# Kernel optimization log

Measured on AMD Instinct MI355X. Metric: run time of the kernel, lower is better.

## Reference

```python
import jax, jax.numpy as jnp
import numpy as np

EPS = 1e-8
NEG_FILL = -9e15


def _normalize(x):
    # matches torch cosine_similarity's norm clamp with eps=1e-8
    n = jnp.sqrt(jnp.sum(x * x, axis=-1, keepdims=True))
    return x / jnp.maximum(n, EPS)


def setup_inputs() -> dict:
    key = jax.random.key(0)
    k1, k2 = jax.random.split(key)
    N, D = 8192, 512
    cxr_feats = jax.random.normal(k1, (N, D), dtype=jnp.float32)
    ehr_feats = jax.random.normal(k2, (N, D), dtype=jnp.float32)
    temperature = jnp.asarray(0.07, dtype=jnp.float32)
    return {"cxr_feats": cxr_feats, "ehr_feats": ehr_feats, "temperature": temperature}


def reference(cxr_feats, ehr_feats, temperature):
    # normalize then GEMM instead of broadcasted [N,N,D] cosine_similarity
    cn = _normalize(cxr_feats)                      # [N, D]
    en = _normalize(ehr_feats)                      # [N, D]
    cos_sim = jnp.einsum('id,jd->ij', cn, en)       # [N, N]
    cos_sim = cos_sim / temperature
    N = cos_sim.shape[0]
    eye = jnp.eye(N, dtype=bool)
    diag = jnp.diagonal(cos_sim)                    # positives
    cos_neg = jnp.where(eye, NEG_FILL, cos_sim)     # mask self-pairs
    nll_1 = diag - jax.nn.logsumexp(cos_neg, axis=1)
    nll_2 = diag - jax.nn.logsumexp(cos_neg, axis=0)
    loss = -jnp.mean(nll_1 + nll_2)
    return loss
```

## Files before the change

kernel.cpp:

```cpp
#include <hip/hip_runtime.h>
#include <hip/hip_bf16.h>
#include <stdint.h>
#include <stddef.h>

#define NROWS 8192
#define DDIM  512
#define TILE  128
#define BKB   128
#define NBLK  (NROWS / TILE)

static_assert(NBLK == 64, "bj extraction assumes 64 col-blocks");

typedef float f32x4 __attribute__((ext_vector_type(4)));
typedef long  v2l  __attribute__((ext_vector_type(2)));

__device__ __forceinline__ void async_copy16(const void* g, void* l) {
    __builtin_amdgcn_global_load_lds(
        (const __attribute__((address_space(1))) uint32_t*)g,
        (__attribute__((address_space(3))) uint32_t*)l,
        16, 0, 0);
}

__global__ __launch_bounds__(256) void prep_kernel(
    const float* __restrict__ CXR, const float* __restrict__ EHR,
    uint32_t* __restrict__ CN8, uint32_t* __restrict__ EN8,
    float* __restrict__ rowsum ,
    float* __restrict__ out)
{
    if (blockIdx.x < 64) {
        rowsum[blockIdx.x * 256 + threadIdx.x] = 0.f;
        if (blockIdx.x == 0 && threadIdx.x == 0) out[0] = 0.f;
    }
    const int half = (blockIdx.x >= 2048);
    const float* X = half ? EHR : CXR;
    uint32_t* Y = half ? EN8 : CN8;
    const int row  = (blockIdx.x & 2047) * 4 + (threadIdx.x >> 6);
    const int lane = threadIdx.x & 63;
    const float* xr = X + (size_t)row * DDIM;
    float4 v0 = ((const float4*)xr)[lane];
    float4 v1 = ((const float4*)xr)[lane + 64];
    float ss = v0.x*v0.x + v0.y*v0.y + v0.z*v0.z + v0.w*v0.w
             + v1.x*v1.x + v1.y*v1.y + v1.z*v1.z + v1.w*v1.w;
    #pragma unroll
    for (int d = 1; d < 64; d <<= 1) ss += __shfl_xor(ss, d);
    const float sc = 1.0f / fmaxf(sqrtf(ss), 1e-8f);
    uint32_t* yr = Y + (size_t)row * (DDIM / 4);
    int w0 = __builtin_amdgcn_cvt_pk_fp8_f32(v0.x*sc, v0.y*sc, 0, false);
    w0     = __builtin_amdgcn_cvt_pk_fp8_f32(v0.z*sc, v0.w*sc, w0, true);
    int w1 = __builtin_amdgcn_cvt_pk_fp8_f32(v1.x*sc, v1.y*sc, 0, false);
    w1     = __builtin_amdgcn_cvt_pk_fp8_f32(v1.z*sc, v1.w*sc, w1, true);
    yr[lane]      = (uint32_t)w0;
    yr[lane + 64] = (uint32_t)w1;
}

__global__ __launch_bounds__(256, 2) void gemm_loss_kernel(
    const uint8_t* __restrict__ A,
    const uint8_t* __restrict__ B,
    const float* __restrict__ temp_p,
    float* __restrict__ rowsum,
    float* __restrict__ colsum,
    float* __restrict__ diagv)
{
    __shared__ uint8_t As[TILE * BKB];
    __shared__ uint8_t Bs[TILE * BKB];

    const int tid  = threadIdx.x;
    const int lane = tid & 63;
    const int wv   = tid >> 6;
    const int wi   = (wv >> 1) * 64;
    const int wj   = (wv & 1) * 64;
    const int lcol = lane & 15;
    const int q    = lane >> 4;

    const int bi = blockIdx.x & (NBLK - 1);
    const int bj = blockIdx.x >> 6;
    const int row0 = bi * TILE;
    const int col0 = bj * TILE;

    const int sr = lane >> 3;
    const int su = (lane & 7) ^ sr;
    const uint8_t* Ag = A + (size_t)(row0 + wv * 32 + sr) * DDIM + su * 16;
    const uint8_t* Bg = B + (size_t)(col0 + wv * 32 + sr) * DDIM + su * 16;

    f32x4 acc[4][4] = {};

    for (int k0 = 0; k0 < DDIM; k0 += BKB) {
        __syncthreads();
        #pragma unroll
        for (int c = 0; c < 4; ++c) {
            async_copy16(Ag + (size_t)(c * 8) * DDIM + k0, &As[(wv * 32 + c * 8) * BKB]);
            async_copy16(Bg + (size_t)(c * 8) * DDIM + k0, &Bs[(wv * 32 + c * 8) * BKB]);
        }
        __syncthreads();

        #pragma unroll
        for (int kk2 = 0; kk2 < 2; ++kk2) {
            const int u = kk2 * 4 + q;
            long aflo[4], afhi[4];
            #pragma unroll
            for (int mt = 0; mt < 4; ++mt) {
                const int r = wi + mt * 16 + lcol;
                v2l a16 = *(const v2l*)&As[r * BKB + (u ^ (r & 7)) * 16];
                aflo[mt] = a16.x; afhi[mt] = a16.y;
            }
            #pragma unroll
            for (int nt = 0; nt < 4; ++nt) {
                const int r = wj + nt * 16 + lcol;
                v2l b16 = *(const v2l*)&Bs[r * BKB + (u ^ (r & 7)) * 16];
                #pragma unroll
                for (int mt = 0; mt < 4; ++mt)
                    acc[mt][nt] = __builtin_amdgcn_mfma_f32_16x16x32_fp8_fp8(
                        aflo[mt], b16.x, acc[mt][nt], 0, 0, 0);
                #pragma unroll
                for (int mt = 0; mt < 4; ++mt)
                    acc[mt][nt] = __builtin_amdgcn_mfma_f32_16x16x32_fp8_fp8(
                        afhi[mt], b16.y, acc[mt][nt], 0, 0, 0);
            }
        }
    }

    const float invT = 1.0f / temp_p[0];
    const float M = invT;

    float rs[4][4];
    float cs[4];
    #pragma unroll
    for (int mt = 0; mt < 4; ++mt)
        #pragma unroll
        for (int r = 0; r < 4; ++r) rs[mt][r] = 0.f;
    #pragma unroll
    for (int nt = 0; nt < 4; ++nt) cs[nt] = 0.f;

    #pragma unroll
    for (int mt = 0; mt < 4; ++mt) {
        #pragma unroll
        for (int nt = 0; nt < 4; ++nt) {
            #pragma unroll
            for (int r = 0; r < 4; ++r) {
                const int gi = row0 + wi + mt * 16 + q * 4 + r;
                const int gj = col0 + wj + nt * 16 + lcol;
                const float sv = acc[mt][nt][r] * invT;
                float e;
                if (gi == gj) { diagv[gi] = sv; e = 0.f; }
                else          { e = __expf(sv - M); }
                rs[mt][r] += e;
                cs[nt]    += e;
            }
        }
    }

    #pragma unroll
    for (int d = 1; d < 16; d <<= 1)
        #pragma unroll
        for (int mt = 0; mt < 4; ++mt)
            #pragma unroll
            for (int r = 0; r < 4; ++r)
                rs[mt][r] += __shfl_xor(rs[mt][r], d);

    #pragma unroll
    for (int d = 16; d < 64; d <<= 1)
        #pragma unroll
        for (int nt = 0; nt < 4; ++nt)
            cs[nt] += __shfl_xor(cs[nt], d);

    if (lcol == 0) {
        #pragma unroll
        for (int mt = 0; mt < 4; ++mt)
            #pragma unroll
            for (int r = 0; r < 4; ++r)
                atomicAdd(&rowsum[row0 + wi + mt * 16 + q * 4 + r], rs[mt][r]);
    }
    if (q == 0) {
        #pragma unroll
        for (int nt = 0; nt < 4; ++nt)
            atomicAdd(&colsum[col0 + wj + nt * 16 + lcol], cs[nt]);
    }
}

__global__ __launch_bounds__(256) void finalize_kernel(
    const float* __restrict__ rowsum, const float* __restrict__ colsum,
    const float* __restrict__ diagv,  const float* __restrict__ temp_p,
    float* __restrict__ out)
{
    __shared__ float red[4];
    const float M = 1.0f / temp_p[0];
    const int i = blockIdx.x * 256 + threadIdx.x;
    float s = 2.f * M + logf(rowsum[i]) + logf(colsum[i]) - 2.f * diagv[i];
    #pragma unroll
    for (int d = 1; d < 64; d <<= 1) s += __shfl_xor(s, d);
    if ((threadIdx.x & 63) == 0) red[threadIdx.x >> 6] = s;
    __syncthreads();
    if (threadIdx.x == 0)
        atomicAdd(out, (red[0] + red[1] + red[2] + red[3]) / (float)NROWS);
}

extern "C" void kernel_launch(void* const* d_in, const int* in_sizes, int n_in,
                              void* d_out, int out_size, void* d_ws, size_t ws_size,
                              hipStream_t stream) {
    (void)in_sizes; (void)n_in; (void)out_size; (void)ws_size;
    const float* cxr    = (const float*)d_in[0];
    const float* ehr    = (const float*)d_in[1];
    const float* temp_p = (const float*)d_in[2];
    float* out = (float*)d_out;

    float* rowsum = (float*)d_ws;
    float* colsum = rowsum + NROWS;
    float* diagv  = colsum + NROWS;
    uint32_t* cn8 = (uint32_t*)(diagv + NROWS);
    uint32_t* en8 = cn8 + (size_t)NROWS * (DDIM / 4);
    const uint8_t* cnb = (const uint8_t*)cn8;
    const uint8_t* enb = (const uint8_t*)en8;

    prep_kernel<<<4096, 256, 0, stream>>>(cxr, ehr, cn8, en8, rowsum, out);
    gemm_loss_kernel<<<NBLK * NBLK, 256, 0, stream>>>(cnb, enb, temp_p, rowsum, colsum, diagv);
    finalize_kernel<<<NROWS / 256, 256, 0, stream>>>(rowsum, colsum, diagv, temp_p, out);
}
```

Baseline: 136.7 us.

## Stage full K in LDS as two halves with 8-wave blocks

The GEMM block grows from 4 to 8 waves, and each wave now computes a 64x32 sub-tile instead of 64x64. The whole 512-wide K panel for A and B is loaded into 128KB of dynamic LDS in two halves. Loads for the second half are issued before computing on the first, which cuts the four-step load/sync loop down to two stages with some overlap. The cost is that the large LDS footprint limits how many blocks fit on each CU. Fewer accumulator registers per wave may offset part of that.

```diff
diff --git a/kernel.cpp b/kernel.cpp
--- a/kernel.cpp
+++ b/kernel.cpp
@@ -6,8 +6,9 @@
 #define NROWS 8192
 #define DDIM  512
 #define TILE  128
-#define BKB   128
+#define KHALF 256
 #define NBLK  (NROWS / TILE)
+#define LDS_BYTES (4 * TILE * KHALF)
 
 static_assert(NBLK == 64, "bj extraction assumes 64 col-blocks");
 
@@ -53,7 +54,7 @@
     yr[lane + 64] = (uint32_t)w1;
 }
 
-__global__ __launch_bounds__(256, 2) void gemm_loss_kernel(
+__global__ __launch_bounds__(512, 2) void gemm_loss_kernel(
     const uint8_t* __restrict__ A,
     const uint8_t* __restrict__ B,
     const float* __restrict__ temp_p,
@@ -61,14 +62,15 @@
     float* __restrict__ colsum,
     float* __restrict__ diagv)
 {
-    __shared__ uint8_t As[TILE * BKB];
-    __shared__ uint8_t Bs[TILE * BKB];
+    extern __shared__ uint8_t smem[];
+    uint8_t* As[2] = { smem,             smem + 2 * TILE * KHALF };
+    uint8_t* Bs[2] = { smem + TILE * KHALF, smem + 3 * TILE * KHALF };
 
     const int tid  = threadIdx.x;
     const int lane = tid & 63;
     const int wv   = tid >> 6;
-    const int wi   = (wv >> 1) * 64;
-    const int wj   = (wv & 1) * 64;
+    const int wi   = (wv & 1) * 64;
+    const int wj   = (wv >> 1) * 32;
     const int lcol = lane & 15;
     const int q    = lane >> 4;
 
@@ -77,36 +79,44 @@
     const int row0 = bi * TILE;
     const int col0 = bj * TILE;
 
-    const int sr = lane >> 3;
-    const int su = (lane & 7) ^ sr;
-    const uint8_t* Ag = A + (size_t)(row0 + wv * 32 + sr) * DDIM + su * 16;
-    const uint8_t* Bg = B + (size_t)(col0 + wv * 32 + sr) * DDIM + su * 16;
-
-    f32x4 acc[4][4] = {};
-
-    for (int k0 = 0; k0 < DDIM; k0 += BKB) {
-        __syncthreads();
+    const int ro = lane >> 4;
+    const uint8_t* Agb = A + (size_t)(row0 + wv * 16 + ro) * DDIM;
+    const uint8_t* Bgb = B + (size_t)(col0 + wv * 16 + ro) * DDIM;
+
+    #pragma unroll
+    for (int s = 0; s < 2; ++s) {
+        if (s == 1) __syncthreads();
         #pragma unroll
         for (int c = 0; c < 4; ++c) {
-            async_copy16(Ag + (size_t)(c * 8) * DDIM + k0, &As[(wv * 32 + c * 8) * BKB]);
-            async_copy16(Bg + (size_t)(c * 8) * DDIM + k0, &Bs[(wv * 32 + c * 8) * BKB]);
+            const int R0 = wv * 16 + c * 4;
+            const int gu = (lane & 15) ^ ((R0 & 4) | ro);
+            const size_t goff = (size_t)(c * 4) * DDIM + s * KHALF + gu * 16;
+            async_copy16(Agb + goff, As[s] + R0 * KHALF + lane * 16);
+            async_copy16(Bgb + goff, Bs[s] + R0 * KHALF + lane * 16);
         }
-        __syncthreads();
-
-        #pragma unroll
-        for (int kk2 = 0; kk2 < 2; ++kk2) {
+    }
+
+    f32x4 acc[4][2] = {};
+    const float invT = 1.0f / temp_p[0];
+    const float M = invT;
+
+    #pragma unroll
+    for (int s = 0; s < 2; ++s) {
+        if (s == 1) __syncthreads();
+        #pragma unroll
+        for (int kk2 = 0; kk2 < 4; ++kk2) {
             const int u = kk2 * 4 + q;
             long aflo[4], afhi[4];
             #pragma unroll
             for (int mt = 0; mt < 4; ++mt) {
                 const int r = wi + mt * 16 + lcol;
-                v2l a16 = *(const v2l*)&As[r * BKB + (u ^ (r & 7)) * 16];
+                v2l a16 = *(const v2l*)&As[s][r * KHALF + (u ^ (r & 7)) * 16];
                 aflo[mt] = a16.x; afhi[mt] = a16.y;
             }
             #pragma unroll
-            for (int nt = 0; nt < 4; ++nt) {
+            for (int nt = 0; nt < 2; ++nt) {
                 const int r = wj + nt * 16 + lcol;
-                v2l b16 = *(const v2l*)&Bs[r * BKB + (u ^ (r & 7)) * 16];
+                v2l b16 = *(const v2l*)&Bs[s][r * KHALF + (u ^ (r & 7)) * 16];
                 #pragma unroll
                 for (int mt = 0; mt < 4; ++mt)
                     acc[mt][nt] = __builtin_amdgcn_mfma_f32_16x16x32_fp8_fp8(
@@ -119,22 +129,18 @@
         }
     }
 
-    const float invT = 1.0f / temp_p[0];
-    const float M = invT;
-
     float rs[4][4];
-    float cs[4];
+    float cs[2];
     #pragma unroll
     for (int mt = 0; mt < 4; ++mt)
         #pragma unroll
         for (int r = 0; r < 4; ++r) rs[mt][r] = 0.f;
-    #pragma unroll
-    for (int nt = 0; nt < 4; ++nt) cs[nt] = 0.f;
+    cs[0] = cs[1] = 0.f;
 
     #pragma unroll
     for (int mt = 0; mt < 4; ++mt) {
         #pragma unroll
-        for (int nt = 0; nt < 4; ++nt) {
+        for (int nt = 0; nt < 2; ++nt) {
             #pragma unroll
             for (int r = 0; r < 4; ++r) {
                 const int gi = row0 + wi + mt * 16 + q * 4 + r;
@@ -160,7 +166,7 @@
     #pragma unroll
     for (int d = 16; d < 64; d <<= 1)
         #pragma unroll
-        for (int nt = 0; nt < 4; ++nt)
+        for (int nt = 0; nt < 2; ++nt)
             cs[nt] += __shfl_xor(cs[nt], d);
 
     if (lcol == 0) {
@@ -172,7 +178,7 @@
     }
     if (q == 0) {
         #pragma unroll
-        for (int nt = 0; nt < 4; ++nt)
+        for (int nt = 0; nt < 2; ++nt)
             atomicAdd(&colsum[col0 + wj + nt * 16 + lcol], cs[nt]);
     }
 }
@@ -211,7 +217,10 @@
     const uint8_t* cnb = (const uint8_t*)cn8;
     const uint8_t* enb = (const uint8_t*)en8;
 
+    hipFuncSetAttribute(reinterpret_cast<const void*>(gemm_loss_kernel),
+                        hipFuncAttributeMaxDynamicSharedMemorySize, LDS_BYTES);
+
     prep_kernel<<<4096, 256, 0, stream>>>(cxr, ehr, cn8, en8, rowsum, out);
-    gemm_loss_kernel<<<NBLK * NBLK, 256, 0, stream>>>(cnb, enb, temp_p, rowsum, colsum, diagv);
+    gemm_loss_kernel<<<NBLK * NBLK, 512, LDS_BYTES, stream>>>(cnb, enb, temp_p, rowsum, colsum, diagv);
     finalize_kernel<<<NROWS / 256, 256, 0, stream>>>(rowsum, colsum, diagv, temp_p, out);
 }
```

Result: slower. 197.4 us (+44.4%).

## Double-buffer LDS tiles with smaller K slices to overlap loads and MFMA

Applied to the files above, without the earlier changes.

Halves the K-slice to 64 bytes and adds two LDS buffers so the async global-to-LDS copy of the next slice is issued before computing on the current one. This replaces the two barriers per slice with one and precomputes the swizzled LDS read offsets. The intent is to hide global load latency behind MFMA work. In exchange there are more loop iterations with less MFMA work per barrier. Correctness relies on the single barrier after compute, which is meant to order the next slice's async copies before they are read.

```diff
diff --git a/kernel.cpp b/kernel.cpp
--- a/kernel.cpp
+++ b/kernel.cpp
@@ -6,7 +6,8 @@
 #define NROWS 8192
 #define DDIM  512
 #define TILE  128
-#define BKB   128
+#define BKB   64
+#define NSTG  (DDIM / BKB)
 #define NBLK  (NROWS / TILE)
 
 static_assert(NBLK == 64, "bj extraction assumes 64 col-blocks");
@@ -61,8 +62,8 @@
     float* __restrict__ colsum,
     float* __restrict__ diagv)
 {
-    __shared__ uint8_t As[TILE * BKB];
-    __shared__ uint8_t Bs[TILE * BKB];
+    __shared__ uint8_t As[2][TILE * BKB];
+    __shared__ uint8_t Bs[2][TILE * BKB];
 
     const int tid  = threadIdx.x;
     const int lane = tid & 63;
@@ -77,46 +78,61 @@
     const int row0 = bi * TILE;
     const int col0 = bj * TILE;
 
-    const int sr = lane >> 3;
-    const int su = (lane & 7) ^ sr;
-    const uint8_t* Ag = A + (size_t)(row0 + wv * 32 + sr) * DDIM + su * 16;
-    const uint8_t* Bg = B + (size_t)(col0 + wv * 32 + sr) * DDIM + su * 16;
+    const int rr = lane >> 2;
+    const int gu = (lane & 3) ^ (rr & 3);
+    const uint8_t* Agb = A + (size_t)(row0 + wv * 32 + rr) * DDIM + gu * 16;
+    const uint8_t* Bgb = B + (size_t)(col0 + wv * 32 + rr) * DDIM + gu * 16;
+
+    int aoff[4], boff[4];
+    #pragma unroll
+    for (int t = 0; t < 4; ++t) {
+        const int ra = wi + t * 16 + lcol;
+        const int rb = wj + t * 16 + lcol;
+        aoff[t] = ra * BKB + ((q ^ (ra & 3)) * 16);
+        boff[t] = rb * BKB + ((q ^ (rb & 3)) * 16);
+    }
 
     f32x4 acc[4][4] = {};
 
-    for (int k0 = 0; k0 < DDIM; k0 += BKB) {
+    #pragma unroll
+    for (int c = 0; c < 2; ++c) {
+        async_copy16(Agb + (size_t)(c * 16) * DDIM, &As[0][(wv * 32 + c * 16) * BKB]);
+        async_copy16(Bgb + (size_t)(c * 16) * DDIM, &Bs[0][(wv * 32 + c * 16) * BKB]);
+    }
+    __syncthreads();
+
+    for (int s = 0; s < NSTG; ++s) {
+        const int cur = s & 1;
+        if (s + 1 < NSTG) {
+            const int nxt = (s + 1) & 1;
+            const int k0 = (s + 1) * BKB;
+            #pragma unroll
+            for (int c = 0; c < 2; ++c) {
+                async_copy16(Agb + (size_t)(c * 16) * DDIM + k0,
+                             &As[nxt][(wv * 32 + c * 16) * BKB]);
+                async_copy16(Bgb + (size_t)(c * 16) * DDIM + k0,
+                             &Bs[nxt][(wv * 32 + c * 16) * BKB]);
+            }
+        }
+        long aflo[4], afhi[4];
+        #pragma unroll
+        for (int mt = 0; mt < 4; ++mt) {
+            v2l a16 = *(const v2l*)&As[cur][aoff[mt]];
+            aflo[mt] = a16.x; afhi[mt] = a16.y;
+        }
+        #pragma unroll
+        for (int nt = 0; nt < 4; ++nt) {
+            v2l b16 = *(const v2l*)&Bs[cur][boff[nt]];
+            #pragma unroll
+            for (int mt = 0; mt < 4; ++mt)
+                acc[mt][nt] = __builtin_amdgcn_mfma_f32_16x16x32_fp8_fp8(
+                    aflo[mt], b16.x, acc[mt][nt], 0, 0, 0);
+            #pragma unroll
+            for (int mt = 0; mt < 4; ++mt)
+                acc[mt][nt] = __builtin_amdgcn_mfma_f32_16x16x32_fp8_fp8(
+                    afhi[mt], b16.y, acc[mt][nt], 0, 0, 0);
+        }
         __syncthreads();
-        #pragma unroll
-        for (int c = 0; c < 4; ++c) {
-            async_copy16(Ag + (size_t)(c * 8) * DDIM + k0, &As[(wv * 32 + c * 8) * BKB]);
-            async_copy16(Bg + (size_t)(c * 8) * DDIM + k0, &Bs[(wv * 32 + c * 8) * BKB]);
-        }
-        __syncthreads();
-
-        #pragma unroll
-        for (int kk2 = 0; kk2 < 2; ++kk2) {
-            const int u = kk2 * 4 + q;
-            long aflo[4], afhi[4];
-            #pragma unroll
-            for (int mt = 0; mt < 4; ++mt) {
-                const int r = wi + mt * 16 + lcol;
-                v2l a16 = *(const v2l*)&As[r * BKB + (u ^ (r & 7)) * 16];
-                aflo[mt] = a16.x; afhi[mt] = a16.y;
-            }
-            #pragma unroll
-            for (int nt = 0; nt < 4; ++nt) {
-                const int r = wj + nt * 16 + lcol;
-                v2l b16 = *(const v2l*)&Bs[r * BKB + (u ^ (r & 7)) * 16];
-                #pragma unroll
-                for (int mt = 0; mt < 4; ++mt)
-                    acc[mt][nt] = __builtin_amdgcn_mfma_f32_16x16x32_fp8_fp8(
-                        aflo[mt], b16.x, acc[mt][nt], 0, 0, 0);
-                #pragma unroll
-                for (int mt = 0; mt < 4; ++mt)
-                    acc[mt][nt] = __builtin_amdgcn_mfma_f32_16x16x32_fp8_fp8(
-                        afhi[mt], b16.y, acc[mt][nt], 0, 0, 0);
-            }
-        }
     }
 
     const float invT = 1.0f / temp_p[0];
```

Measured after the change: 142.3 us. +4.0%, slower.

## Double-buffer B tile in LDS and load A fragments directly into registers

Applied to the files above, without the earlier changes.

The GEMM main loop now loads A operand fragments straight from global memory into registers instead of staging them through LDS. B tiles are double-buffered in LDS with async copies issued one K-step ahead, and the next A fragments are prefetched into registers while the current step's MFMAs run. The aim is to overlap global loads with compute and halve LDS traffic and barriers. In exchange it uses more registers, which may hurt occupancy at launch bounds of 2, and each wave issues uncoalesced-ish 16-byte global loads for A that are duplicated across waves sharing rows.

```diff
diff --git a/kernel.cpp b/kernel.cpp
--- a/kernel.cpp
+++ b/kernel.cpp
@@ -61,8 +61,7 @@
     float* __restrict__ colsum,
     float* __restrict__ diagv)
 {
-    __shared__ uint8_t As[TILE * BKB];
-    __shared__ uint8_t Bs[TILE * BKB];
+    __shared__ uint8_t Bs[2][TILE * BKB];
 
     const int tid  = threadIdx.x;
     const int lane = tid & 63;
@@ -79,43 +78,73 @@
 
     const int sr = lane >> 3;
     const int su = (lane & 7) ^ sr;
-    const uint8_t* Ag = A + (size_t)(row0 + wv * 32 + sr) * DDIM + su * 16;
     const uint8_t* Bg = B + (size_t)(col0 + wv * 32 + sr) * DDIM + su * 16;
 
+    const uint8_t* aptr[4];
+    #pragma unroll
+    for (int mt = 0; mt < 4; ++mt)
+        aptr[mt] = A + (size_t)(row0 + wi + mt * 16 + lcol) * DDIM + q * 16;
+
+    int boff[2][4];
+    #pragma unroll
+    for (int kk2 = 0; kk2 < 2; ++kk2)
+        #pragma unroll
+        for (int nt = 0; nt < 4; ++nt) {
+            const int r = wj + nt * 16 + lcol;
+            boff[kk2][nt] = r * BKB + (((kk2 * 4 + q) ^ (r & 7)) * 16);
+        }
+
     f32x4 acc[4][4] = {};
 
-    for (int k0 = 0; k0 < DDIM; k0 += BKB) {
-        __syncthreads();
-        #pragma unroll
-        for (int c = 0; c < 4; ++c) {
-            async_copy16(Ag + (size_t)(c * 8) * DDIM + k0, &As[(wv * 32 + c * 8) * BKB]);
-            async_copy16(Bg + (size_t)(c * 8) * DDIM + k0, &Bs[(wv * 32 + c * 8) * BKB]);
-        }
-        __syncthreads();
-
+    #pragma unroll
+    for (int c = 0; c < 4; ++c)
+        async_copy16(Bg + (size_t)(c * 8) * DDIM, &Bs[0][(wv * 32 + c * 8) * BKB]);
+    v2l areg[2][4];
+    #pragma unroll
+    for (int kk2 = 0; kk2 < 2; ++kk2)
+        #pragma unroll
+        for (int mt = 0; mt < 4; ++mt)
+            areg[kk2][mt] = *(const v2l*)(aptr[mt] + kk2 * 64);
+    __syncthreads();
+
+    #pragma unroll
+    for (int s = 0; s < 4; ++s) {
+        const int cur = s & 1;
+        v2l anew[2][4];
+        if (s < 3) {
+            const int k1 = (s + 1) * BKB;
+            #pragma unroll
+            for (int c = 0; c < 4; ++c)
+                async_copy16(Bg + (size_t)(c * 8) * DDIM + k1,
+                             &Bs[cur ^ 1][(wv * 32 + c * 8) * BKB]);
+            #pragma unroll
+            for (int kk2 = 0; kk2 < 2; ++kk2)
+                #pragma unroll
+                for (int mt = 0; mt < 4; ++mt)
+                    anew[kk2][mt] = *(const v2l*)(aptr[mt] + k1 + kk2 * 64);
+        }
         #pragma unroll
         for (int kk2 = 0; kk2 < 2; ++kk2) {
-            const int u = kk2 * 4 + q;
-            long aflo[4], afhi[4];
-            #pragma unroll
-            for (int mt = 0; mt < 4; ++mt) {
-                const int r = wi + mt * 16 + lcol;
-                v2l a16 = *(const v2l*)&As[r * BKB + (u ^ (r & 7)) * 16];
-                aflo[mt] = a16.x; afhi[mt] = a16.y;
+            #pragma unroll
+            for (int nt = 0; nt < 4; ++nt) {
+                v2l b16 = *(const v2l*)&Bs[cur][boff[kk2][nt]];
+                #pragma unroll
+                for (int mt = 0; mt < 4; ++mt)
+                    acc[mt][nt] = __builtin_amdgcn_mfma_f32_16x16x32_fp8_fp8(
+                        areg[kk2][mt].x, b16.x, acc[mt][nt], 0, 0, 0);
+                #pragma unroll
+                for (int mt = 0; mt < 4; ++mt)
+                    acc[mt][nt] = __builtin_amdgcn_mfma_f32_16x16x32_fp8_fp8(
+                        areg[kk2][mt].y, b16.y, acc[mt][nt], 0, 0, 0);
             }
-            #pragma unroll
-            for (int nt = 0; nt < 4; ++nt) {
-                const int r = wj + nt * 16 + lcol;
-                v2l b16 = *(const v2l*)&Bs[r * BKB + (u ^ (r & 7)) * 16];
-                #pragma unroll
-                for (int mt = 0; mt < 4; ++mt)
-                    acc[mt][nt] = __builtin_amdgcn_mfma_f32_16x16x32_fp8_fp8(
-                        aflo[mt], b16.x, acc[mt][nt], 0, 0, 0);
-                #pragma unroll
-                for (int mt = 0; mt < 4; ++mt)
-                    acc[mt][nt] = __builtin_amdgcn_mfma_f32_16x16x32_fp8_fp8(
-                        afhi[mt], b16.y, acc[mt][nt], 0, 0, 0);
-            }
+        }
+        if (s < 3) {
+            __syncthreads();
+            #pragma unroll
+            for (int kk2 = 0; kk2 < 2; ++kk2)
+                #pragma unroll
+                for (int mt = 0; mt < 4; ++mt)
+                    areg[kk2][mt] = anew[kk2][mt];
         }
     }
 
```

After: 161.1 us. +17.8%, slower.
